# Performance work log

Measured on AMD Instinct MI355X. Metric: run time of the kernel, lower is better.

## Reference

```python
import jax, jax.numpy as jnp
import numpy as np

B = 10      # number of interacting objects
NDIM = 2    # self.n: position/velocity dimensionality

# Edge list equivalent to rel_rec/rel_send one-hot matrices (edges grouped by receiver)
_rec_idx, _send_idx = np.where(~np.eye(B, dtype=bool))


def _mlp(x, W0, b0, W1, b1, W2, b2):
    # MLP with 2 hidden softplus layers, linear output
    h = jax.nn.softplus(x @ W0 + b0)
    h = jax.nn.softplus(h @ W1 + b1)
    return h @ W2 + b2


def setup_inputs() -> dict:
    key = jax.random.key(0)
    ks = jax.random.split(key, 7)
    N = 8192            # trajectories per batch
    H = 128             # hidden width of self-dynamics MLP
    Hi = 128            # hidden width of interaction MLP
    nin = 2 * NDIM      # self MLP input dim (pos+vel)
    nout = 2 * NDIM     # n_f_out for order=1
    nin_i = 3 * NDIM    # interaction MLP input dim (p1-p2, v1, v2)
    w = lambda k, shp: jax.random.normal(k, shp, jnp.float32) / np.float32(np.sqrt(shp[0]))
    return {
        "z": jax.random.normal(ks[0], (N * B, 2 * NDIM), jnp.float32),
        "fW0": w(ks[1], (nin, H)),   "fb0": jnp.zeros((H,), jnp.float32),
        "fW1": w(ks[2], (H, H)),     "fb1": jnp.zeros((H,), jnp.float32),
        "fW2": w(ks[3], (H, nout)),  "fb2": jnp.zeros((nout,), jnp.float32),
        "iW0": w(ks[4], (nin_i, Hi)),"ib0": jnp.zeros((Hi,), jnp.float32),
        "iW1": w(ks[5], (Hi, Hi)),   "ib1": jnp.zeros((Hi,), jnp.float32),
        "iW2": w(ks[6], (Hi, nout)), "ib2": jnp.zeros((nout,), jnp.float32),
    }


def reference(z, fW0, fb0, fW1, fb1, fW2, fb2, iW0, ib0, iW1, ib1, iW2, ib2):
    # One evaluation of the ODE vector field (order=1, n_aug_dyn=n_aug_st=0).
    n = NDIM
    NB = z.shape[0]
    N = NB // B
    dz_self = _mlp(z, fW0, fb0, fW1, fb1, fW2, fb2)            # [N*B, 2n]
    z3 = z.reshape(N, B, 2 * n)
    recv = z3[:, _rec_idx]                                     # [N, B(B-1), 2n] gather (node2edge)
    send = z3[:, _send_idx]
    # odefint input: (p_recv - p_send, v_recv, v_send)  -> [N, B(B-1), 3n]
    inp = jnp.concatenate([recv[..., :n] - send[..., :n], recv[..., n:], send[..., n:]], -1)
    dz_int = _mlp(inp, iW0, ib0, iW1, ib1, iW2, ib2)           # [N, B(B-1), 2n]
    dz_int = dz_int.reshape(N, B, B - 1, 2 * n).sum(2)         # sum over senders per receiver
    dz = dz_self.reshape(N, B, 2 * n) + dz_int
    return dz.reshape(NB, 2 * n)
```

## Files before the change

### kernel.cpp

```cpp
#include <hip/hip_runtime.h>
#include <hip/hip_bf16.h>

#define NDIM 2
#define BB 10
#define H 128
#define PAIRS 90
#define MROWS 128
#define LDH 132
#define UST 136
#define LOG2E 1.4426950408889634f
#define LN2   0.6931471805599453f

typedef short short8 __attribute__((ext_vector_type(8)));
typedef short short4v __attribute__((ext_vector_type(4)));
typedef float floatx4 __attribute__((ext_vector_type(4)));
typedef float floatx16 __attribute__((ext_vector_type(16)));

__device__ inline short f2bf(float x) {
    unsigned u = __float_as_uint(x);
    return (short)((u + 0x7fffu + ((u >> 16) & 1u)) >> 16);
}

#if __has_builtin(__builtin_amdgcn_cvt_pk_bf16_f32)
typedef __bf16 bf16x2_t __attribute__((ext_vector_type(2)));
__device__ inline unsigned pk2(float a, float b) {
    bf16x2_t v = __builtin_amdgcn_cvt_pk_bf16_f32(a, b);
    return __builtin_bit_cast(unsigned, v);
}
#else
__device__ inline unsigned pk2(float a, float b) {
    unsigned ua = __float_as_uint(a), ub = __float_as_uint(b);
    ua = (ua + 0x7fffu + ((ua >> 16) & 1u)) >> 16;
    ub = (ub + 0x7fffu + ((ub >> 16) & 1u)) & 0xffff0000u;
    return ua | ub;
}
#endif

__device__ inline float sp2(float xs) {
    float m = fmaxf(xs, 0.f);
#if __has_builtin(__builtin_amdgcn_exp2f)
    float t = __builtin_amdgcn_exp2f(-fabsf(xs));
#else
    float t = exp2f(-fabsf(xs));
#endif
    float q = fmaf(t, fmaf(t, 0.2057f, -0.6484f), 1.4426950f);
    return fmaf(t, q, m) * LN2;
}

__device__ inline float blo(unsigned d) { return __uint_as_float(d << 16); }
__device__ inline float bhif(unsigned d) { return __uint_as_float(d & 0xffff0000u); }

__device__ inline short8 ld8(const short* p) {
    short4v lo = *(const short4v*)p;
    short4v hi = *(const short4v*)(p + 4);
    return short8{lo[0], lo[1], lo[2], lo[3], hi[0], hi[1], hi[2], hi[3]};
}

__global__ void prep_weights(const float* __restrict__ iW1, const float* __restrict__ fW1,
                             const float* __restrict__ iW2, const float* __restrict__ fW2,
                             const float* __restrict__ ib1, const float* __restrict__ fb1,
                             const float* __restrict__ iW0, const float* __restrict__ ib0,
                             const float* __restrict__ fW0, const float* __restrict__ fb0,
                             short* __restrict__ W1Fi, short* __restrict__ W1Ff,
                             short* __restrict__ W2Fi, short* __restrict__ W2Ff,
                             float* __restrict__ scal) {
    int t = blockIdx.x * blockDim.x + threadIdx.x;
    int stride = gridDim.x * blockDim.x;
    for (int fidx = t; fidx < 16384; fidx += stride) {
        int j = fidx & 7, lane = (fidx >> 3) & 63, nt = (fidx >> 9) & 3, ks = fidx >> 11;
        int k = 16 * ks + ((lane >> 5) << 3) + j;
        int n = 32 * nt + (lane & 31);
        W1Fi[fidx] = f2bf(iW1[k * H + n] * LOG2E);
        W1Ff[fidx] = f2bf(fW1[k * H + n] * LOG2E);
    }
    for (int fidx = t; fidx < 2048; fidx += stride) {
        int j = fidx & 7, lane = (fidx >> 3) & 63, ks = fidx >> 9;
        int k = 32 * ks + ((lane >> 4) << 3) + j;
        int n = lane & 15;
        W2Fi[fidx] = (n < 4) ? f2bf(iW2[k * 4 + n]) : (short)0;
        W2Ff[fidx] = (n < 4) ? f2bf(fW2[k * 4 + n]) : (short)0;
    }
    if (t < 128) {
        scal[t] = ib1[t] * LOG2E;
        scal[128 + t] = fb1[t] * LOG2E;
        scal[1024 + t] = ib0[t] * LOG2E;
        scal[1664 + t] = fb0[t] * LOG2E;
    }
    if (t < 768) scal[256 + t] = iW0[t] * LOG2E;
    if (t < 512) scal[1152 + t] = fW0[t] * LOG2E;
}

__global__ __launch_bounds__(512, 8) void fused_kernel(
    const float* __restrict__ z,
    const float* __restrict__ ib2, const float* __restrict__ fb2,
    const short* __restrict__ W1Fi, const short* __restrict__ W2Fi,
    const short* __restrict__ W1Ff, const short* __restrict__ W2Ff,
    const float* __restrict__ scal, float* __restrict__ out) {
    __shared__ __align__(16) short h0s[MROWS * LDH];
    __shared__ __align__(16) short uwsb[2 * BB * UST];
    __shared__ __align__(16) float4 zs4[BB];
    short* usb = uwsb;
    short* wsb = uwsb + BB * UST;
    float* outs = (float*)uwsb;

    int n = blockIdx.x;
    int tid = threadIdx.x, lane = tid & 63, wave = tid >> 6;
    int c31 = lane & 31, halfk = lane >> 5;
    int ntw = wave & 3, mhalf = wave >> 2;

    if (tid < BB) zs4[tid] = ((const float4*)z)[n * BB + tid];
    __syncthreads();

    {
        const float* iW0s = scal + 256;
        for (int u = tid; u < 640; u += 512) {
            int b = u >> 6, c2 = (u & 63) * 2;
            float4 zb = zs4[b];
            float2 p0 = *(const float2*)(iW0s + c2);
            float2 p1 = *(const float2*)(iW0s + 128 + c2);
            float2 p2 = *(const float2*)(iW0s + 256 + c2);
            float2 p3 = *(const float2*)(iW0s + 384 + c2);
            float2 p4 = *(const float2*)(iW0s + 512 + c2);
            float2 p5 = *(const float2*)(iW0s + 640 + c2);
            float2 pb = *(const float2*)(scal + 1024 + c2);
            float s0 = zb.x * p0.x + zb.y * p1.x;
            float s1 = zb.x * p0.y + zb.y * p1.y;
            float u0 = pb.x + s0 + zb.z * p2.x + zb.w * p3.x;
            float u1 = pb.y + s1 + zb.z * p2.y + zb.w * p3.y;
            float w0 = -s0 + zb.z * p4.x + zb.w * p5.x;
            float w1 = -s1 + zb.z * p4.y + zb.w * p5.y;
            *(unsigned*)(usb + b * UST + c2) = pk2(u0, u1);
            *(unsigned*)(wsb + b * UST + c2) = pk2(w0, w1);
        }
    }
    if (tid < 320) {
        int b = tid >> 5, c4 = (tid & 31) * 4;
        const float* fW0s = scal + 1152;
        float4 zb = zs4[b];
        float4 q0 = *(const float4*)(fW0s + c4);
        float4 q1 = *(const float4*)(fW0s + 128 + c4);
        float4 q2 = *(const float4*)(fW0s + 256 + c4);
        float4 q3 = *(const float4*)(fW0s + 384 + c4);
        float4 qb = *(const float4*)(scal + 1664 + c4);
        float a0 = qb.x + zb.x * q0.x + zb.y * q1.x + zb.z * q2.x + zb.w * q3.x;
        float a1 = qb.y + zb.x * q0.y + zb.y * q1.y + zb.z * q2.y + zb.w * q3.y;
        float a2 = qb.z + zb.x * q0.z + zb.y * q1.z + zb.z * q2.z + zb.w * q3.z;
        float a3 = qb.w + zb.x * q0.w + zb.y * q1.w + zb.z * q2.w + zb.w * q3.w;
        uint2 pk;
        pk.x = pk2(sp2(a0), sp2(a1));
        pk.y = pk2(sp2(a2), sp2(a3));
        *(uint2*)(h0s + (96 + b) * LDH + c4) = pk;
    }
    for (int t = tid; t < 726; t += 512) {
        int r = 106 + t / 33, d2 = (t % 33) * 4;
        *(uint2*)(h0s + r * LDH + d2) = uint2{0u, 0u};
    }
    __syncthreads();

    {
        int m0 = tid >> 4, c8 = (tid & 15) * 8;
#pragma unroll
        for (int t = 0; t < 3; ++t) {
            int m = m0 + 32 * t;
            uint2 o0 = {0u, 0u}, o1 = {0u, 0u};
            if (m < PAIRS) {
                int i = (m * 57) >> 9;
                int s = m - 9 * i;
                int j = s + (s >= i);
                uint4 uu = *(const uint4*)(usb + i * UST + c8);
                uint4 ww = *(const uint4*)(wsb + j * UST + c8);
                float x0 = blo(uu.x) + blo(ww.x), x1 = bhif(uu.x) + bhif(ww.x);
                float x2 = blo(uu.y) + blo(ww.y), x3 = bhif(uu.y) + bhif(ww.y);
                float x4 = blo(uu.z) + blo(ww.z), x5 = bhif(uu.z) + bhif(ww.z);
                float x6 = blo(uu.w) + blo(ww.w), x7 = bhif(uu.w) + bhif(ww.w);
                o0.x = pk2(sp2(x0), sp2(x1));
                o0.y = pk2(sp2(x2), sp2(x3));
                o1.x = pk2(sp2(x4), sp2(x5));
                o1.y = pk2(sp2(x6), sp2(x7));
            }
            *(uint2*)(h0s + m * LDH + c8) = o0;
            *(uint2*)(h0s + m * LDH + c8 + 4) = o1;
        }
    }
    __syncthreads();

    int hb = 32 * ntw + 4 * halfk;
    floatx16 acc0, acc1;
    {
        const float* blo_ = scal;
        const float* bhi_ = mhalf ? (scal + 128) : scal;
#pragma unroll
        for (int g = 0; g < 4; ++g) {
            float4 v0 = *(const float4*)(blo_ + hb + 8 * g);
            float4 v1 = *(const float4*)(bhi_ + hb + 8 * g);
            acc0[4 * g + 0] = v0.x; acc0[4 * g + 1] = v0.y;
            acc0[4 * g + 2] = v0.z; acc0[4 * g + 3] = v0.w;
            acc1[4 * g + 0] = v1.x; acc1[4 * g + 1] = v1.y;
            acc1[4 * g + 2] = v1.z; acc1[4 * g + 3] = v1.w;
        }
    }
    int rowA = 64 * mhalf + c31;
    int rowB = rowA + 32;
    {
        const short* WA = W1Fi + (ntw * 64 + lane) * 8;
        short8 a_cur = *(const short8*)WA;
#pragma unroll
        for (int ks = 0; ks < 8; ++ks) {
            short8 a_nxt = a_cur;
            if (ks < 7) a_nxt = *(const short8*)(WA + (ks + 1) * 2048);
            short8 bf = ld8(h0s + rowA * LDH + 16 * ks + 8 * halfk);
            acc0 = __builtin_amdgcn_mfma_f32_32x32x16_bf16(a_cur, bf, acc0, 0, 0, 0);
            a_cur = a_nxt;
        }
    }
    {
        const short* WB = (mhalf ? W1Ff : W1Fi) + (ntw * 64 + lane) * 8;
        short8 a_cur = *(const short8*)WB;
#pragma unroll
        for (int ks = 0; ks < 8; ++ks) {
            short8 a_nxt = a_cur;
            if (ks < 7) a_nxt = *(const short8*)(WB + (ks + 1) * 2048);
            short8 bf = ld8(h0s + rowB * LDH + 16 * ks + 8 * halfk);
            acc1 = __builtin_amdgcn_mfma_f32_32x32x16_bf16(a_cur, bf, acc1, 0, 0, 0);
            a_cur = a_nxt;
        }
    }
    __syncthreads();

#pragma unroll
    for (int g = 0; g < 4; ++g) {
        uint2 pa, pb;
        pa.x = pk2(sp2(acc0[4 * g + 0]), sp2(acc0[4 * g + 1]));
        pa.y = pk2(sp2(acc0[4 * g + 2]), sp2(acc0[4 * g + 3]));
        pb.x = pk2(sp2(acc1[4 * g + 0]), sp2(acc1[4 * g + 1]));
        pb.y = pk2(sp2(acc1[4 * g + 2]), sp2(acc1[4 * g + 3]));
        *(uint2*)(h0s + rowA * LDH + 32 * ntw + 8 * g + 4 * halfk) = pa;
        *(uint2*)(h0s + rowB * LDH + 32 * ntw + 8 * g + 4 * halfk) = pb;
    }
    __syncthreads();

    {
        int rit = lane & 15, quad = lane >> 4;
        if (wave < 7) {
            const short* W2 = (wave == 6) ? W2Ff : W2Fi;
            const float* b2 = (wave == 6) ? fb2 : ib2;
            floatx4 a = {0.f, 0.f, 0.f, 0.f};
            if (quad == 0) {
                float4 bbv = *(const float4*)b2;
                a = floatx4{bbv.x, bbv.y, bbv.z, bbv.w};
            }
#pragma unroll
            for (int ks = 0; ks < 4; ++ks) {
                short8 w2v = *(const short8*)(W2 + (ks * 64 + lane) * 8);
                short8 bf = ld8(h0s + (16 * wave + rit) * LDH + 32 * ks + quad * 8);
                a = __builtin_amdgcn_mfma_f32_16x16x32_bf16(w2v, bf, a, 0, 0, 0);
            }
            if (quad == 0) {
                float4 o = {a[0], a[1], a[2], a[3]};
                *(float4*)(outs + (16 * wave + rit) * 4) = o;
            }
        }
    }
    __syncthreads();

    if (tid < BB * 4) {
        int i = tid >> 2, c = tid & 3;
        float s = outs[(96 + i) * 4 + c];
#pragma unroll
        for (int p = 0; p < 9; ++p) s += outs[(9 * i + p) * 4 + c];
        out[(n * BB + i) * 4 + c] = s;
    }
}

extern "C" void kernel_launch(void* const* d_in, const int* in_sizes, int n_in,
                              void* d_out, int out_size, void* d_ws, size_t ws_size,
                              hipStream_t stream) {
    const float* z   = (const float*)d_in[0];
    const float* fW0 = (const float*)d_in[1];
    const float* fb0 = (const float*)d_in[2];
    const float* fW1 = (const float*)d_in[3];
    const float* fb1 = (const float*)d_in[4];
    const float* fW2 = (const float*)d_in[5];
    const float* fb2 = (const float*)d_in[6];
    const float* iW0 = (const float*)d_in[7];
    const float* ib0 = (const float*)d_in[8];
    const float* iW1 = (const float*)d_in[9];
    const float* ib1 = (const float*)d_in[10];
    const float* iW2 = (const float*)d_in[11];
    const float* ib2 = (const float*)d_in[12];
    float* out = (float*)d_out;

    short* wsS = (short*)d_ws;
    short* W1Fi = wsS;
    short* W1Ff = wsS + 16384;
    short* W2Fi = wsS + 32768;
    short* W2Ff = wsS + 34816;
    float* scal = (float*)(wsS + 36864);

    int NB = in_sizes[0] / (2 * NDIM);
    int Nsys = NB / BB;

    hipLaunchKernelGGL(prep_weights, dim3(128), dim3(256), 0, stream,
                       iW1, fW1, iW2, fW2, ib1, fb1, iW0, ib0, fW0, fb0,
                       W1Fi, W1Ff, W2Fi, W2Ff, scal);
    hipLaunchKernelGGL(fused_kernel, dim3(Nsys), dim3(512), 0, stream,
                       z, ib2, fb2, W1Fi, W2Fi, W1Ff, W2Ff, scal, out);
}
```

Baseline: 191.0 us.

## Widen LDS row stride for 16B loads and preload W1 fragments into registers

Changes the LDS row stride from 132 to 136 shorts so every row starts on a 16-byte boundary. This lets the MFMA operand reads and the hidden-layer writes use single 128-bit LDS accesses instead of pairs of 64-bit ones, and simplifies the zero-padding loop. All eight W1 A-fragments are now loaded from global memory at kernel start, so their latency overlaps the layer-0 work; the self-MLP half reloads from W1Ff between the two MMA passes. Holding the fragments costs extra VGPRs, and the occupancy hint drops from 8 to 6 to allow for that, which may reduce the number of resident waves.

```diff
diff --git a/kernel.cpp b/kernel.cpp
--- a/kernel.cpp
+++ b/kernel.cpp
@@ -6,13 +6,12 @@
 #define H 128
 #define PAIRS 90
 #define MROWS 128
-#define LDH 132
+#define LDH 136
 #define UST 136
 #define LOG2E 1.4426950408889634f
 #define LN2   0.6931471805599453f
 
 typedef short short8 __attribute__((ext_vector_type(8)));
-typedef short short4v __attribute__((ext_vector_type(4)));
 typedef float floatx4 __attribute__((ext_vector_type(4)));
 typedef float floatx16 __attribute__((ext_vector_type(16)));
 
@@ -49,12 +48,6 @@
 
 __device__ inline float blo(unsigned d) { return __uint_as_float(d << 16); }
 __device__ inline float bhif(unsigned d) { return __uint_as_float(d & 0xffff0000u); }
-
-__device__ inline short8 ld8(const short* p) {
-    short4v lo = *(const short4v*)p;
-    short4v hi = *(const short4v*)(p + 4);
-    return short8{lo[0], lo[1], lo[2], lo[3], hi[0], hi[1], hi[2], hi[3]};
-}
 
 __global__ void prep_weights(const float* __restrict__ iW1, const float* __restrict__ fW1,
                              const float* __restrict__ iW2, const float* __restrict__ fW2,
@@ -90,7 +83,7 @@
     if (t < 512) scal[1152 + t] = fW0[t] * LOG2E;
 }
 
-__global__ __launch_bounds__(512, 8) void fused_kernel(
+__global__ __launch_bounds__(512, 6) void fused_kernel(
     const float* __restrict__ z,
     const float* __restrict__ ib2, const float* __restrict__ fb2,
     const short* __restrict__ W1Fi, const short* __restrict__ W2Fi,
@@ -107,6 +100,11 @@
     int tid = threadIdx.x, lane = tid & 63, wave = tid >> 6;
     int c31 = lane & 31, halfk = lane >> 5;
     int ntw = wave & 3, mhalf = wave >> 2;
+
+    short8 af[8];
+#pragma unroll
+    for (int ks = 0; ks < 8; ++ks)
+        af[ks] = *(const short8*)(W1Fi + ((ks * 4 + ntw) * 64 + lane) * 8);
 
     if (tid < BB) zs4[tid] = ((const float4*)z)[n * BB + tid];
     __syncthreads();
@@ -151,9 +149,9 @@
         pk.y = pk2(sp2(a2), sp2(a3));
         *(uint2*)(h0s + (96 + b) * LDH + c4) = pk;
     }
-    for (int t = tid; t < 726; t += 512) {
-        int r = 106 + t / 33, d2 = (t % 33) * 4;
-        *(uint2*)(h0s + r * LDH + d2) = uint2{0u, 0u};
+    if (tid < 352) {
+        int r = 106 + (tid >> 4), c8 = (tid & 15) * 8;
+        *(uint4*)(h0s + r * LDH + c8) = uint4{0u, 0u, 0u, 0u};
     }
     __syncthreads();
 
@@ -162,7 +160,7 @@
 #pragma unroll
         for (int t = 0; t < 3; ++t) {
             int m = m0 + 32 * t;
-            uint2 o0 = {0u, 0u}, o1 = {0u, 0u};
+            uint4 o = {0u, 0u, 0u, 0u};
             if (m < PAIRS) {
                 int i = (m * 57) >> 9;
                 int s = m - 9 * i;
@@ -173,13 +171,12 @@
                 float x2 = blo(uu.y) + blo(ww.y), x3 = bhif(uu.y) + bhif(ww.y);
                 float x4 = blo(uu.z) + blo(ww.z), x5 = bhif(uu.z) + bhif(ww.z);
                 float x6 = blo(uu.w) + blo(ww.w), x7 = bhif(uu.w) + bhif(ww.w);
-                o0.x = pk2(sp2(x0), sp2(x1));
-                o0.y = pk2(sp2(x2), sp2(x3));
-                o1.x = pk2(sp2(x4), sp2(x5));
-                o1.y = pk2(sp2(x6), sp2(x7));
-            }
-            *(uint2*)(h0s + m * LDH + c8) = o0;
-            *(uint2*)(h0s + m * LDH + c8 + 4) = o1;
+                o.x = pk2(sp2(x0), sp2(x1));
+                o.y = pk2(sp2(x2), sp2(x3));
+                o.z = pk2(sp2(x4), sp2(x5));
+                o.w = pk2(sp2(x6), sp2(x7));
+            }
+            *(uint4*)(h0s + m * LDH + c8) = o;
         }
     }
     __syncthreads();
@@ -201,29 +198,20 @@
     }
     int rowA = 64 * mhalf + c31;
     int rowB = rowA + 32;
-    {
-        const short* WA = W1Fi + (ntw * 64 + lane) * 8;
-        short8 a_cur = *(const short8*)WA;
-#pragma unroll
-        for (int ks = 0; ks < 8; ++ks) {
-            short8 a_nxt = a_cur;
-            if (ks < 7) a_nxt = *(const short8*)(WA + (ks + 1) * 2048);
-            short8 bf = ld8(h0s + rowA * LDH + 16 * ks + 8 * halfk);
-            acc0 = __builtin_amdgcn_mfma_f32_32x32x16_bf16(a_cur, bf, acc0, 0, 0, 0);
-            a_cur = a_nxt;
-        }
-    }
-    {
-        const short* WB = (mhalf ? W1Ff : W1Fi) + (ntw * 64 + lane) * 8;
-        short8 a_cur = *(const short8*)WB;
-#pragma unroll
-        for (int ks = 0; ks < 8; ++ks) {
-            short8 a_nxt = a_cur;
-            if (ks < 7) a_nxt = *(const short8*)(WB + (ks + 1) * 2048);
-            short8 bf = ld8(h0s + rowB * LDH + 16 * ks + 8 * halfk);
-            acc1 = __builtin_amdgcn_mfma_f32_32x32x16_bf16(a_cur, bf, acc1, 0, 0, 0);
-            a_cur = a_nxt;
-        }
+#pragma unroll
+    for (int ks = 0; ks < 8; ++ks) {
+        short8 bf = *(const short8*)(h0s + rowA * LDH + 16 * ks + 8 * halfk);
+        acc0 = __builtin_amdgcn_mfma_f32_32x32x16_bf16(af[ks], bf, acc0, 0, 0, 0);
+    }
+    if (mhalf) {
+#pragma unroll
+        for (int ks = 0; ks < 8; ++ks)
+            af[ks] = *(const short8*)(W1Ff + ((ks * 4 + ntw) * 64 + lane) * 8);
+    }
+#pragma unroll
+    for (int ks = 0; ks < 8; ++ks) {
+        short8 bf = *(const short8*)(h0s + rowB * LDH + 16 * ks + 8 * halfk);
+        acc1 = __builtin_amdgcn_mfma_f32_32x32x16_bf16(af[ks], bf, acc1, 0, 0, 0);
     }
     __syncthreads();
 
@@ -252,7 +240,7 @@
 #pragma unroll
             for (int ks = 0; ks < 4; ++ks) {
                 short8 w2v = *(const short8*)(W2 + (ks * 64 + lane) * 8);
-                short8 bf = ld8(h0s + (16 * wave + rit) * LDH + 32 * ks + quad * 8);
+                short8 bf = *(const short8*)(h0s + (16 * wave + rit) * LDH + 32 * ks + quad * 8);
                 a = __builtin_amdgcn_mfma_f32_16x16x32_bf16(w2v, bf, a, 0, 0, 0);
             }
             if (quad == 0) {
```

Result: faster. 184.4 us (-3.5%).
